# Kernel tuning notes

Measured on AMD Instinct MI355X. Metric: run time of the kernel, lower is better.

The kernel has to match this reference:

```python
import jax, jax.numpy as jnp
import numpy as np
import math

NUM_HEADS = 16
QK_NOPE = 128
QK_ROPE = 64
V_DIM = 128
Q_HEAD_DIM = QK_NOPE + QK_ROPE  # 192
KV_LORA = 512
ROPE_THETA = 10000.0
EPS = 1e-6


def setup_inputs() -> dict:
    key = jax.random.key(0)
    ks = jax.random.split(key, 8)
    B, S, H = 2, 2048, 2048
    hidden_states = jax.random.normal(ks[0], (B, S, H), dtype=jnp.float32)
    position_ids = jnp.broadcast_to(jnp.arange(S, dtype=jnp.int64), (B, S))
    attention_mask = jnp.broadcast_to(jnp.tril(jnp.ones((S, S), dtype=bool)), (B, 1, S, S))
    sc = 0.02
    w_q_down = jax.random.normal(ks[1], (1536, H), dtype=jnp.float32) * sc
    q_norm_w = jnp.ones((1536,), dtype=jnp.float32)
    w_q_up = jax.random.normal(ks[2], (NUM_HEADS * Q_HEAD_DIM, 1536), dtype=jnp.float32) * sc
    w_kv_down = jax.random.normal(ks[3], (KV_LORA + QK_ROPE, H), dtype=jnp.float32) * sc
    kv_norm_w = jnp.ones((KV_LORA,), dtype=jnp.float32)
    w_kv_up = jax.random.normal(ks[4], (NUM_HEADS * (QK_NOPE + V_DIM), KV_LORA), dtype=jnp.float32) * sc
    w_out = jax.random.normal(ks[5], (H, NUM_HEADS * V_DIM), dtype=jnp.float32) * sc
    return {"hidden_states": hidden_states, "position_ids": position_ids,
            "attention_mask": attention_mask, "w_q_down": w_q_down, "q_norm_w": q_norm_w,
            "w_q_up": w_q_up, "w_kv_down": w_kv_down, "kv_norm_w": kv_norm_w,
            "w_kv_up": w_kv_up, "w_out": w_out}


def rms_norm(x, w):
    xf = x.astype(jnp.float32)
    var = jnp.mean(xf * xf, axis=-1, keepdims=True)
    return w * (xf * jax.lax.rsqrt(var + EPS)).astype(x.dtype)


def rotate_half(x):
    d = x.shape[-1]
    return jnp.concatenate((-x[..., d // 2:], x[..., :d // 2]), axis=-1)


def _deinterleave(x):
    # torch: view(..., d//2, 2).transpose(-1,-2).reshape(..., d)
    d = x.shape[-1]
    return x.reshape(*x.shape[:-1], d // 2, 2).swapaxes(-1, -2).reshape(*x.shape[:-1], d)


def _rope_tables(seq_len, dtype):
    inv_freq = 1.0 / (ROPE_THETA ** (jnp.arange(0, QK_ROPE, 2, dtype=jnp.float32) / QK_ROPE))
    t = jnp.arange(seq_len, dtype=jnp.float32)
    freqs = jnp.outer(t, inv_freq)          # [S, QK_ROPE//2]
    emb = jnp.concatenate((freqs, freqs), axis=-1)  # [S, QK_ROPE]
    return jnp.cos(emb).astype(dtype), jnp.sin(emb).astype(dtype)


def mla_forward(hidden_states, position_ids, attention_mask,
                w_q_down, q_norm_w, w_q_up, w_kv_down, kv_norm_w, w_kv_up, w_out):
    B, S, H = hidden_states.shape
    # low-rank Q path
    q = hidden_states @ w_q_down.T                   # [B,S,1536]
    q = rms_norm(q, q_norm_w)
    q = q @ w_q_up.T                                 # [B,S,NH*192]
    q = q.reshape(B, S, NUM_HEADS, Q_HEAD_DIM).transpose(0, 2, 1, 3)  # [B,NH,S,192]
    q_nope, q_rope = q[..., :QK_NOPE], q[..., QK_NOPE:]
    # low-rank KV path
    c = hidden_states @ w_kv_down.T                  # [B,S,576]
    c_kv, k_rope = c[..., :KV_LORA], c[..., KV_LORA:]
    k_rope = k_rope.reshape(B, S, 1, QK_ROPE).transpose(0, 2, 1, 3)   # [B,1,S,64]
    kv = rms_norm(c_kv, kv_norm_w) @ w_kv_up.T       # [B,S,NH*(128+128)]
    kv = kv.reshape(B, S, NUM_HEADS, QK_NOPE + V_DIM).transpose(0, 2, 1, 3)
    k_nope, v = kv[..., :QK_NOPE], kv[..., QK_NOPE:]  # [B,NH,S,128] each
    # decoupled RoPE on the rope sub-dim
    cos, sin = _rope_tables(S, hidden_states.dtype)
    cos_p = cos[position_ids][:, None]               # [B,1,S,64]
    sin_p = sin[position_ids][:, None]
    qr = _deinterleave(q_rope)
    kr = _deinterleave(k_rope)
    q_rope = qr * cos_p + rotate_half(qr) * sin_p
    k_rope = kr * cos_p + rotate_half(kr) * sin_p
    query = jnp.concatenate([q_nope, q_rope], axis=-1)                      # [B,NH,S,192]
    key = jnp.concatenate([k_nope, jnp.broadcast_to(k_rope, (B, NUM_HEADS, S, QK_ROPE))], axis=-1)
    scores = jnp.einsum('bhqd,bhkd->bhqk', query, key) / math.sqrt(Q_HEAD_DIM)
    scores = jnp.where(attention_mask, scores, -jnp.inf)
    attn = jax.nn.softmax(scores, axis=-1).astype(query.dtype)              # [B,NH,S,S]
    out = jnp.einsum('bhqk,bhkd->bhqd', attn, v)                            # [B,NH,S,128]
    out = out.transpose(0, 2, 1, 3).reshape(B, S, NUM_HEADS * V_DIM)
    out = out @ w_out.T                                                     # [B,S,H]
    return out, attn


def reference(hidden_states, position_ids, attention_mask,
              w_q_down, q_norm_w, w_q_up, w_kv_down, kv_norm_w, w_kv_up, w_out):
    return mla_forward(hidden_states, position_ids, attention_mask,
                       w_q_down, q_norm_w, w_q_up, w_kv_down, kv_norm_w, w_kv_up, w_out)
```

## Files before the change

### kernel.cpp

```cpp
#include <hip/hip_runtime.h>
#include <hip/hip_bf16.h>
#include <math.h>

typedef unsigned short u16;
typedef unsigned int u32;
typedef __bf16 bf16x8 __attribute__((ext_vector_type(8)));
typedef float f32x4 __attribute__((ext_vector_type(4)));

__device__ __forceinline__ float bf2f(u16 h) {
    return __uint_as_float(((u32)h) << 16);
}
__device__ __forceinline__ u16 f2bf(float f) {
    u32 u = __float_as_uint(f);
    u32 r = (u + 0x7fffu + ((u >> 16) & 1u)) >> 16;
    return (u16)r;
}

__device__ __forceinline__ f32x4 mfma16(bf16x8 a, bf16x8 b, f32x4 c) {
    return __builtin_amdgcn_mfma_f32_16x16x32_bf16(a, b, c, 0, 0, 0);
}

__device__ __forceinline__ void g2l(const u16* g, u16* l) {
    __builtin_amdgcn_global_load_lds(
        (const __attribute__((address_space(1))) unsigned int*)g,
        (__attribute__((address_space(3))) unsigned int*)l,
        16, 0, 0);
}

struct DetectArgs {
    const void* p[8];
    int n[8];
};

__global__ __launch_bounds__(256) void detect_k(DetectArgs a, u32* flags) {
    int b = blockIdx.x;
    int t = threadIdx.x;
    const u16* p = (const u16*)a.p[b];
    u16 v = p[2 * t];
    int e = (v >> 7) & 0xff;
    bool insane = (e < 87) || (e > 167);
    unsigned long long m = __ballot(insane);
    __shared__ u32 s[4];
    int w = t >> 6;
    if ((t & 63) == 0) s[w] = (m != 0ull) ? 1u : 0u;
    __syncthreads();
    if (t == 0) flags[b] = s[0] | s[1] | s[2] | s[3];
}

__global__ __launch_bounds__(256) void convert_k(
    const void* src, u16* dst, int n, const u32* flags, int fi)
{
    u32 f = flags[fi];
    int j0 = blockIdx.x * 1024 + threadIdx.x * 4;
    if (f) {
        const float* s = (const float*)src;
        for (int k = 0; k < 4; k++) {
            int j = j0 + k;
            if (j < n) dst[j] = f2bf(s[j]);
        }
    } else {
        const u16* s = (const u16*)src;
        for (int k = 0; k < 4; k++) {
            int j = j0 + k;
            if (j < n) dst[j] = s[j];
        }
    }
}

__global__ __launch_bounds__(256) void gemm128(
    const u16* __restrict__ X, int xRow, long long xBat,
    const u16* __restrict__ W, int wRow, long long wBat,
    u16* __restrict__ Cb, float* __restrict__ Cf,
    int cRow, long long cBatB, long long cBatH,
    int N, int K)
{
    __shared__ __align__(16) u16 As[128 * 32];
    __shared__ __align__(16) u16 Bs[128 * 32];

    int z = blockIdx.z;
    const u16* Xz = X + (long long)z * xBat;
    const u16* Wz = W + (long long)z * wBat;
    long long cOff = (long long)(z >> 4) * cBatB + (long long)(z & 15) * cBatH;

    int t = threadIdx.x;
    int lane = t & 63, w = t >> 6;
    int sr = t >> 2;
    int sc = (t & 3) * 8;
    int m0 = blockIdx.y * 128, n0 = blockIdx.x * 128;
    int wr = (w >> 1) * 64, wc = (w & 1) * 64;
    int mrow = lane & 15, quad = lane >> 4;

    u16* As0 = &As[t * 8];
    u16* As1 = &As[2048 + t * 8];
    u16* Bs0 = &Bs[t * 8];
    u16* Bs1 = &Bs[2048 + t * 8];

    f32x4 zero = {0.f, 0.f, 0.f, 0.f};
    f32x4 acc[4][4];
    for (int i = 0; i < 4; i++)
        for (int j = 0; j < 4; j++) acc[i][j] = zero;

    for (int k0 = 0; k0 < K; k0 += 32) {
        const u16* ga0 = Xz + (long long)(m0 + sr) * xRow + k0 + sc;
        const u16* ga1 = ga0 + (long long)64 * xRow;
        int bn0 = n0 + sr;      if (bn0 >= N) bn0 = N - 1;
        int bn1 = n0 + sr + 64; if (bn1 >= N) bn1 = N - 1;
        const u16* gb0 = Wz + (long long)bn0 * wRow + k0 + sc;
        const u16* gb1 = Wz + (long long)bn1 * wRow + k0 + sc;
        __syncthreads();
        g2l(ga0, As0);
        g2l(ga1, As1);
        g2l(gb0, Bs0);
        g2l(gb1, Bs1);
        __syncthreads();

        bf16x8 af[4], bfr[4];
        for (int i = 0; i < 4; i++) {
            af[i]  = *(const bf16x8*)(&As[(wr + i * 16 + mrow) * 32 + quad * 8]);
            bfr[i] = *(const bf16x8*)(&Bs[(wc + i * 16 + mrow) * 32 + quad * 8]);
        }
        for (int mt = 0; mt < 4; mt++)
            for (int nt = 0; nt < 4; nt++)
                acc[mt][nt] = mfma16(af[mt], bfr[nt], acc[mt][nt]);
    }

    for (int mt = 0; mt < 4; mt++)
        for (int nt = 0; nt < 4; nt++)
            for (int r = 0; r < 4; r++) {
                int row = m0 + wr + mt * 16 + quad * 4 + r;
                int col = n0 + wc + nt * 16 + mrow;
                if (col < N) {
                    long long idx = cOff + (long long)row * cRow + col;
                    float v = acc[mt][nt][r];
                    if (Cb) Cb[idx] = f2bf(v); else Cf[idx] = v;
                }
            }
}

__global__ __launch_bounds__(256) void gemm128_xf32(
    const float* __restrict__ X, int xRow, long long xBat,
    const u16* __restrict__ W, int wRow, long long wBat,
    u16* __restrict__ Cb, int cRow, long long cBatB, long long cBatH,
    int N, int K)
{
    __shared__ __align__(16) u16 As[128 * 32];
    __shared__ __align__(16) u16 Bs[128 * 32];

    int z = blockIdx.z;
    const float* Xz = X + (long long)z * xBat;
    const u16* Wz = W + (long long)z * wBat;
    long long cOff = (long long)(z >> 4) * cBatB + (long long)(z & 15) * cBatH;

    int t = threadIdx.x;
    int lane = t & 63, w = t >> 6;
    int sr = t >> 2;
    int sc = (t & 3) * 8;
    int m0 = blockIdx.y * 128, n0 = blockIdx.x * 128;
    int wr = (w >> 1) * 64, wc = (w & 1) * 64;
    int mrow = lane & 15, quad = lane >> 4;

    u16* Bs0 = &Bs[t * 8];
    u16* Bs1 = &Bs[2048 + t * 8];

    f32x4 zero = {0.f, 0.f, 0.f, 0.f};
    f32x4 acc[4][4];
    for (int i = 0; i < 4; i++)
        for (int j = 0; j < 4; j++) acc[i][j] = zero;

    int kEnd = m0 + 128; if (kEnd > K) kEnd = K;

    for (int k0 = 0; k0 < kEnd; k0 += 32) {
        const float* ap0 = Xz + (long long)(m0 + sr) * xRow + k0 + sc;
        const float* ap1 = Xz + (long long)(m0 + sr + 64) * xRow + k0 + sc;
        float4 a0l = *(const float4*)(ap0), a0h = *(const float4*)(ap0 + 4);
        float4 a1l = *(const float4*)(ap1), a1h = *(const float4*)(ap1 + 4);
        int bn0 = n0 + sr;      if (bn0 >= N) bn0 = N - 1;
        int bn1 = n0 + sr + 64; if (bn1 >= N) bn1 = N - 1;
        const u16* gb0 = Wz + (long long)bn0 * wRow + k0 + sc;
        const u16* gb1 = Wz + (long long)bn1 * wRow + k0 + sc;
        u16 pa0[8] = {f2bf(a0l.x), f2bf(a0l.y), f2bf(a0l.z), f2bf(a0l.w),
                      f2bf(a0h.x), f2bf(a0h.y), f2bf(a0h.z), f2bf(a0h.w)};
        u16 pa1[8] = {f2bf(a1l.x), f2bf(a1l.y), f2bf(a1l.z), f2bf(a1l.w),
                      f2bf(a1h.x), f2bf(a1h.y), f2bf(a1h.z), f2bf(a1h.w)};
        __syncthreads();
        *(uint4*)(&As[sr * 32 + sc]) = *(const uint4*)pa0;
        *(uint4*)(&As[(sr + 64) * 32 + sc]) = *(const uint4*)pa1;
        g2l(gb0, Bs0);
        g2l(gb1, Bs1);
        __syncthreads();

        bf16x8 af[4], bfr[4];
        for (int i = 0; i < 4; i++) {
            af[i]  = *(const bf16x8*)(&As[(wr + i * 16 + mrow) * 32 + quad * 8]);
            bfr[i] = *(const bf16x8*)(&Bs[(wc + i * 16 + mrow) * 32 + quad * 8]);
        }
        for (int mt = 0; mt < 4; mt++)
            for (int nt = 0; nt < 4; nt++)
                acc[mt][nt] = mfma16(af[mt], bfr[nt], acc[mt][nt]);
    }

    for (int mt = 0; mt < 4; mt++)
        for (int nt = 0; nt < 4; nt++)
            for (int r = 0; r < 4; r++) {
                int row = m0 + wr + mt * 16 + quad * 4 + r;
                int col = n0 + wc + nt * 16 + mrow;
                if (col < N)
                    Cb[cOff + (long long)row * cRow + col] = f2bf(acc[mt][nt][r]);
            }
}

__global__ __launch_bounds__(256) void rmsnorm_k(
    const float* __restrict__ in, int inRow,
    const u16* __restrict__ wgt,
    u16* __restrict__ out, int outRow, int len)
{
    int row = blockIdx.x;
    const float* x = in + (long long)row * inRow;
    u16* o = out + (long long)row * outRow;
    int t = threadIdx.x;
    float ss = 0.f;
    for (int j = t; j < len; j += 256) { float v = x[j]; ss += v * v; }
    for (int s = 1; s < 64; s <<= 1) ss += __shfl_xor(ss, s);
    __shared__ float red[4];
    int w = t >> 6, lane = t & 63;
    if (lane == 0) red[w] = ss;
    __syncthreads();
    float tot = red[0] + red[1] + red[2] + red[3];
    float r = rsqrtf(tot / (float)len + 1e-6f);
    for (int j = t; j < len; j += 256)
        o[j] = f2bf(bf2f(wgt[j]) * (x[j] * r));
}

__device__ __forceinline__ void rope64(const float* xin, float* xo, int pos) {
    for (int i = 0; i < 32; i++) {
        float ex = (float)(2 * i) * (1.0f / 64.0f);
        float invf = expf(-ex * 9.210340371976184f);
        float ang = (float)pos * invf;
        float sn, cs;
        sincosf(ang, &sn, &cs);
        float a = xin[2 * i], b = xin[2 * i + 1];
        xo[i] = a * cs - b * sn;
        xo[32 + i] = b * cs + a * sn;
    }
}

__global__ __launch_bounds__(256) void rope_q_k(u16* __restrict__ qf) {
    int idx = blockIdx.x * 256 + threadIdx.x;
    int row = idx >> 4, h = idx & 15, pos = row & 2047;
    u16* p = qf + (long long)row * 3072 + h * 192 + 128;
    float xin[64], xo[64];
    for (int j = 0; j < 64; j++) xin[j] = bf2f(p[j]);
    rope64(xin, xo, pos);
    for (int j = 0; j < 64; j++) p[j] = f2bf(xo[j]);
}

__global__ __launch_bounds__(256) void rope_kk(
    const float* __restrict__ cpre, u16* __restrict__ kr) {
    int row = blockIdx.x * 256 + threadIdx.x;
    int pos = row & 2047;
    const float* src = cpre + (long long)row * 576 + 512;
    float xin[64], xo[64];
    for (int j = 0; j < 64; j++) xin[j] = src[j];
    rope64(xin, xo, pos);
    u16* dst = kr + (long long)row * 64;
    for (int j = 0; j < 64; j++) dst[j] = f2bf(xo[j]);
}

__global__ void transpose_v(const u16* __restrict__ kvup, u16* __restrict__ Vt) {
    __shared__ u16 tile[32][33];
    int bh = blockIdx.z, b = bh >> 4, h = bh & 15;
    int s0 = blockIdx.x * 32, d0 = blockIdx.y * 32;
    int tx = threadIdx.x, ty = threadIdx.y;
    for (int i = 0; i < 4; i++) {
        int s = s0 + ty + i * 8;
        tile[ty + i * 8][tx] = kvup[(long long)(b * 2048 + s) * 4096 + h * 256 + 128 + d0 + tx];
    }
    __syncthreads();
    for (int i = 0; i < 4; i++) {
        int d = d0 + ty + i * 8;
        Vt[((long long)bh * 128 + d) * 2048 + s0 + tx] = tile[tx][ty + i * 8];
    }
}

#define ATTN_SCALE 0.07216878364870323f

__global__ __launch_bounds__(256) void scores_gemm(
    const u16* __restrict__ qf, const u16* __restrict__ kvup,
    const u16* __restrict__ krope, float* __restrict__ attn)
{
    int n0 = blockIdx.x * 128, q0 = blockIdx.y * 128;
    if (n0 > q0) return;
    int bh = blockIdx.z, b = bh >> 4, h = bh & 15;
    const u16* qb = qf + (long long)b * 2048 * 3072 + h * 192;
    const u16* kn = kvup + (long long)b * 2048 * 4096 + h * 256;
    const u16* kr = krope + (long long)b * 2048 * 64;
    long long abase = (long long)bh * 4194304;

    __shared__ __align__(16) u16 As[128 * 32];
    __shared__ __align__(16) u16 Bs[128 * 32];
    int t = threadIdx.x, lane = t & 63, w = t >> 6;
    int sr = t >> 2, sc = (t & 3) * 8;
    int wr = (w >> 1) * 64, wc = (w & 1) * 64;
    int mrow = lane & 15, quad = lane >> 4;

    u16* As0 = &As[t * 8];
    u16* As1 = &As[2048 + t * 8];
    u16* Bs0 = &Bs[t * 8];
    u16* Bs1 = &Bs[2048 + t * 8];

    f32x4 zero = {0.f, 0.f, 0.f, 0.f};
    f32x4 acc[4][4];
    for (int i = 0; i < 4; i++)
        for (int j = 0; j < 4; j++) acc[i][j] = zero;

    for (int k0 = 0; k0 < 192; k0 += 32) {
        const u16* ga0 = qb + (long long)(q0 + sr) * 3072 + k0 + sc;
        const u16* ga1 = ga0 + (long long)64 * 3072;
        const u16 *gb0, *gb1;
        if (k0 < 128) {
            gb0 = kn + (long long)(n0 + sr) * 4096 + k0 + sc;
            gb1 = gb0 + (long long)64 * 4096;
        } else {
            gb0 = kr + (long long)(n0 + sr) * 64 + (k0 - 128) + sc;
            gb1 = gb0 + (long long)64 * 64;
        }
        __syncthreads();
        g2l(ga0, As0);
        g2l(ga1, As1);
        g2l(gb0, Bs0);
        g2l(gb1, Bs1);
        __syncthreads();

        bf16x8 af[4], bfr[4];
        for (int i = 0; i < 4; i++) {
            af[i]  = *(const bf16x8*)(&As[(wr + i * 16 + mrow) * 32 + quad * 8]);
            bfr[i] = *(const bf16x8*)(&Bs[(wc + i * 16 + mrow) * 32 + quad * 8]);
        }
        for (int mt = 0; mt < 4; mt++)
            for (int nt = 0; nt < 4; nt++)
                acc[mt][nt] = mfma16(af[mt], bfr[nt], acc[mt][nt]);
    }

    for (int mt = 0; mt < 4; mt++)
        for (int nt = 0; nt < 4; nt++)
            for (int r = 0; r < 4; r++) {
                int row = q0 + wr + mt * 16 + quad * 4 + r;
                int col = n0 + wc + nt * 16 + mrow;
                attn[abase + (long long)row * 2048 + col] = acc[mt][nt][r] * ATTN_SCALE;
            }
}

__global__ __launch_bounds__(256) void softmax_rows(float* __restrict__ attn) {
    int r = blockIdx.x;
    long long bh = blockIdx.y;
    float* p = attn + bh * 4194304LL + (long long)r * 2048;
    int t = threadIdx.x;
    int valid = r + 1;
    int j0 = t * 4;

    float v[8];
    float mx = -INFINITY;
#pragma unroll
    for (int h = 0; h < 2; h++) {
        int j = j0 + h * 1024;
        if (j + 4 <= valid) {
            float4 q = *(const float4*)(p + j);
            v[h * 4 + 0] = q.x; v[h * 4 + 1] = q.y;
            v[h * 4 + 2] = q.z; v[h * 4 + 3] = q.w;
        } else {
#pragma unroll
            for (int k = 0; k < 4; k++) {
                int jj = j + k;
                v[h * 4 + k] = (jj < valid) ? p[jj] : -INFINITY;
            }
        }
#pragma unroll
        for (int k = 0; k < 4; k++) mx = fmaxf(mx, v[h * 4 + k]);
    }
    for (int s = 1; s < 64; s <<= 1) mx = fmaxf(mx, __shfl_xor(mx, s));
    __shared__ float sm[4], s2[4];
    int w = t >> 6;
    if ((t & 63) == 0) sm[w] = mx;
    __syncthreads();
    mx = fmaxf(fmaxf(sm[0], sm[1]), fmaxf(sm[2], sm[3]));

    float ss = 0.f;
#pragma unroll
    for (int i = 0; i < 8; i++) {
        float e = (v[i] == -INFINITY) ? 0.f : expf(v[i] - mx);
        v[i] = e;
        ss += e;
    }
    for (int s = 1; s < 64; s <<= 1) ss += __shfl_xor(ss, s);
    if ((t & 63) == 0) s2[w] = ss;
    __syncthreads();
    ss = s2[0] + s2[1] + s2[2] + s2[3];
    float inv = 1.0f / ss;

#pragma unroll
    for (int h = 0; h < 2; h++) {
        float4 q;
        q.x = v[h * 4 + 0] * inv;
        q.y = v[h * 4 + 1] * inv;
        q.z = v[h * 4 + 2] * inv;
        q.w = v[h * 4 + 3] * inv;
        *(float4*)(p + j0 + h * 1024) = q;
    }
}

extern "C" void kernel_launch(void* const* d_in, const int* in_sizes, int n_in,
                              void* d_out, int out_size, void* d_ws, size_t ws_size,
                              hipStream_t stream) {
    (void)in_sizes; (void)n_in; (void)out_size; (void)ws_size;

    const void* r_hidden = d_in[0];
    const void* r_wqd    = d_in[3];
    const void* r_qnw    = d_in[4];
    const void* r_wqu    = d_in[5];
    const void* r_wkvd   = d_in[6];
    const void* r_kvnw   = d_in[7];
    const void* r_wkvu   = d_in[8];
    const void* r_wout   = d_in[9];

    float* out_p  = (float*)d_out;
    float* attn_p = (float*)d_out + 8388608LL;

    char* ws = (char*)d_ws;
    size_t off = 0;
    auto alloc = [&](size_t bytes) { void* p = ws + off; off = (off + bytes + 255) & ~(size_t)255; return p; };

    u32* flags = (u32*)alloc(256);
    char* regionA = (char*)alloc(25165824 + 9437184);
    float* q_pre = (float*)regionA;
    float* c_pre = (float*)(regionA + 25165824);
    u16* kv_up   = (u16*)regionA;
    char* regionB = (char*)alloc(16777216);
    u16* hidden_c = (u16*)regionB;
    u16* Vt       = (u16*)regionB;
    char* regionC = (char*)alloc(12582912);
    u16* q_c   = (u16*)regionC;
    u16* kv_c  = (u16*)regionC;
    u16* krope = (u16*)(regionC + 4194304);
    u16* wqd_c  = (u16*)alloc(1536LL * 2048 * 2);
    u16* qnw_c  = (u16*)alloc(1536LL * 2);
    u16* wqu_c  = (u16*)alloc(3072LL * 1536 * 2);
    u16* wkvd_c = (u16*)alloc(576LL * 2048 * 2);
    u16* kvnw_c = (u16*)alloc(512LL * 2);
    u16* wkvu_c = (u16*)alloc(4096LL * 512 * 2);
    u16* wout_c = (u16*)alloc(2048LL * 2048 * 2);
    u16* q_full = (u16*)alloc(4096LL * 3072 * 2);
    u16* Obuf   = q_full;

    DetectArgs da;
    da.p[0] = r_hidden; da.n[0] = 8388608;
    da.p[1] = r_wqd;    da.n[1] = 3145728;
    da.p[2] = r_qnw;    da.n[2] = 1536;
    da.p[3] = r_wqu;    da.n[3] = 4718592;
    da.p[4] = r_wkvd;   da.n[4] = 1179648;
    da.p[5] = r_kvnw;   da.n[5] = 512;
    da.p[6] = r_wkvu;   da.n[6] = 2097152;
    da.p[7] = r_wout;   da.n[7] = 4194304;
    hipLaunchKernelGGL(detect_k, dim3(8), dim3(256), 0, stream, da, flags);

    const void* srcs[8] = {r_hidden, r_wqd, r_qnw, r_wqu, r_wkvd, r_kvnw, r_wkvu, r_wout};
    u16* dsts[8] = {hidden_c, wqd_c, qnw_c, wqu_c, wkvd_c, kvnw_c, wkvu_c, wout_c};
    for (int i = 0; i < 8; i++) {
        int n = da.n[i];
        hipLaunchKernelGGL(convert_k, dim3((n + 1023) / 1024), dim3(256), 0, stream,
            srcs[i], dsts[i], n, flags, i);
    }

    hipLaunchKernelGGL(gemm128, dim3(12, 32, 1), dim3(256), 0, stream,
        hidden_c, 2048, 0LL, wqd_c, 2048, 0LL, (u16*)nullptr, q_pre, 1536, 0LL, 0LL, 1536, 2048);
    hipLaunchKernelGGL(rmsnorm_k, dim3(4096), dim3(256), 0, stream,
        q_pre, 1536, qnw_c, q_c, 1536, 1536);
    hipLaunchKernelGGL(gemm128, dim3(24, 32, 1), dim3(256), 0, stream,
        q_c, 1536, 0LL, wqu_c, 1536, 0LL, q_full, (float*)nullptr, 3072, 0LL, 0LL, 3072, 1536);
    hipLaunchKernelGGL(rope_q_k, dim3(256), dim3(256), 0, stream, q_full);
    hipLaunchKernelGGL(gemm128, dim3(5, 32, 1), dim3(256), 0, stream,
        hidden_c, 2048, 0LL, wkvd_c, 2048, 0LL, (u16*)nullptr, c_pre, 576, 0LL, 0LL, 576, 2048);
    hipLaunchKernelGGL(rmsnorm_k, dim3(4096), dim3(256), 0, stream,
        c_pre, 576, kvnw_c, kv_c, 512, 512);
    hipLaunchKernelGGL(rope_kk, dim3(16), dim3(256), 0, stream, c_pre, krope);
    hipLaunchKernelGGL(gemm128, dim3(32, 32, 1), dim3(256), 0, stream,
        kv_c, 512, 0LL, wkvu_c, 512, 0LL, kv_up, (float*)nullptr, 4096, 0LL, 0LL, 4096, 512);
    hipLaunchKernelGGL(transpose_v, dim3(64, 4, 32), dim3(32, 8), 0, stream, kv_up, Vt);
    hipLaunchKernelGGL(scores_gemm, dim3(16, 16, 32), dim3(256), 0, stream,
        q_full, kv_up, krope, attn_p);
    hipLaunchKernelGGL(softmax_rows, dim3(2048, 32), dim3(256), 0, stream, attn_p);
    hipLaunchKernelGGL(gemm128_xf32, dim3(1, 16, 32), dim3(256), 0, stream,
        attn_p, 2048, 4194304LL, Vt, 2048, 262144LL, Obuf,
        2048, 4194304LL, 128LL, 128, 2048);
    hipLaunchKernelGGL(gemm128, dim3(16, 32, 1), dim3(256), 0, stream,
        Obuf, 2048, 0LL, wout_c, 2048, 0LL, (u16*)nullptr, out_p, 2048, 0LL, 0LL, 2048, 2048);
}
```

Baseline: 1.317 ms.

## Batch converts, merge down-projections and up-projections, zero masked tiles in scores kernel

Replaces the eight conversion launches with one kernel that looks up its segment by block index. Concatenates the q and kv down-projection weights into one GEMM, fuses both RMSNorms into one launch, and runs both up-projection GEMMs in a single dual launch. The scores kernel now writes zeros for fully masked tiles, and softmax stores only the columns up to the causal tile boundary, so the attention matrix is written once instead of twice. Also reverses row order in the attn@V GEMM so the long causal rows are scheduled first, and vectorises the rope loads and stores. The cost is extra workspace aliasing and more branching inside the combined kernels.

```diff
diff --git a/kernel.cpp b/kernel.cpp
--- a/kernel.cpp
+++ b/kernel.cpp
@@ -47,11 +47,23 @@
     if (t == 0) flags[b] = s[0] | s[1] | s[2] | s[3];
 }
 
-__global__ __launch_bounds__(256) void convert_k(
-    const void* src, u16* dst, int n, const u32* flags, int fi)
-{
-    u32 f = flags[fi];
-    int j0 = blockIdx.x * 1024 + threadIdx.x * 4;
+struct ConvArgs {
+    const void* src[8];
+    u16* dst[8];
+    int n[8];
+    int pre[9];
+};
+
+__global__ __launch_bounds__(256) void convert_all(ConvArgs a, const u32* flags) {
+    int bx = blockIdx.x;
+    int i = 0;
+    while (i < 7 && bx >= a.pre[i + 1]) i++;
+    int lb = bx - a.pre[i];
+    int n = a.n[i];
+    u32 f = flags[i];
+    const void* src = a.src[i];
+    u16* dst = a.dst[i];
+    int j0 = lb * 1024 + threadIdx.x * 4;
     if (f) {
         const float* s = (const float*)src;
         for (int k = 0; k < 4; k++) {
@@ -137,6 +149,73 @@
             }
 }
 
+struct DualGemm {
+    const u16* X[2]; int xRow[2];
+    const u16* W[2]; int wRow[2];
+    u16* C[2];       int cRow[2];
+    int N[2]; int K[2]; int xmax[2];
+};
+
+__global__ __launch_bounds__(256) void gemm128_dual(DualGemm d) {
+    int s = blockIdx.z;
+    if ((int)blockIdx.x >= d.xmax[s]) return;
+    const u16* __restrict__ X = d.X[s]; int xRow = d.xRow[s];
+    const u16* __restrict__ W = d.W[s]; int wRow = d.wRow[s];
+    u16* __restrict__ Cb = d.C[s];      int cRow = d.cRow[s];
+    int N = d.N[s], K = d.K[s];
+
+    __shared__ __align__(16) u16 As[128 * 32];
+    __shared__ __align__(16) u16 Bs[128 * 32];
+
+    int t = threadIdx.x;
+    int lane = t & 63, w = t >> 6;
+    int sr = t >> 2;
+    int sc = (t & 3) * 8;
+    int m0 = blockIdx.y * 128, n0 = blockIdx.x * 128;
+    int wr = (w >> 1) * 64, wc = (w & 1) * 64;
+    int mrow = lane & 15, quad = lane >> 4;
+
+    u16* As0 = &As[t * 8];
+    u16* As1 = &As[2048 + t * 8];
+    u16* Bs0 = &Bs[t * 8];
+    u16* Bs1 = &Bs[2048 + t * 8];
+
+    f32x4 zero = {0.f, 0.f, 0.f, 0.f};
+    f32x4 acc[4][4];
+    for (int i = 0; i < 4; i++)
+        for (int j = 0; j < 4; j++) acc[i][j] = zero;
+
+    for (int k0 = 0; k0 < K; k0 += 32) {
+        const u16* ga0 = X + (long long)(m0 + sr) * xRow + k0 + sc;
+        const u16* ga1 = ga0 + (long long)64 * xRow;
+        const u16* gb0 = W + (long long)(n0 + sr) * wRow + k0 + sc;
+        const u16* gb1 = gb0 + (long long)64 * wRow;
+        __syncthreads();
+        g2l(ga0, As0);
+        g2l(ga1, As1);
+        g2l(gb0, Bs0);
+        g2l(gb1, Bs1);
+        __syncthreads();
+
+        bf16x8 af[4], bfr[4];
+        for (int i = 0; i < 4; i++) {
+            af[i]  = *(const bf16x8*)(&As[(wr + i * 16 + mrow) * 32 + quad * 8]);
+            bfr[i] = *(const bf16x8*)(&Bs[(wc + i * 16 + mrow) * 32 + quad * 8]);
+        }
+        for (int mt = 0; mt < 4; mt++)
+            for (int nt = 0; nt < 4; nt++)
+                acc[mt][nt] = mfma16(af[mt], bfr[nt], acc[mt][nt]);
+    }
+
+    for (int mt = 0; mt < 4; mt++)
+        for (int nt = 0; nt < 4; nt++)
+            for (int r = 0; r < 4; r++) {
+                int row = m0 + wr + mt * 16 + quad * 4 + r;
+                int col = n0 + wc + nt * 16 + mrow;
+                Cb[(long long)row * cRow + col] = f2bf(acc[mt][nt][r]);
+            }
+}
+
 __global__ __launch_bounds__(256) void gemm128_xf32(
     const float* __restrict__ X, int xRow, long long xBat,
     const u16* __restrict__ W, int wRow, long long wBat,
@@ -155,7 +234,8 @@
     int lane = t & 63, w = t >> 6;
     int sr = t >> 2;
     int sc = (t & 3) * 8;
-    int m0 = blockIdx.y * 128, n0 = blockIdx.x * 128;
+    int m0 = ((int)gridDim.y - 1 - (int)blockIdx.y) * 128;
+    int n0 = blockIdx.x * 128;
     int wr = (w >> 1) * 64, wc = (w & 1) * 64;
     int mrow = lane & 15, quad = lane >> 4;
 
@@ -209,14 +289,23 @@
             }
 }
 
-__global__ __launch_bounds__(256) void rmsnorm_k(
-    const float* __restrict__ in, int inRow,
-    const u16* __restrict__ wgt,
-    u16* __restrict__ out, int outRow, int len)
+__global__ __launch_bounds__(256) void rmsnorm2_k(
+    const float* __restrict__ base,
+    const u16* __restrict__ qw, const u16* __restrict__ kw,
+    u16* __restrict__ qo, u16* __restrict__ ko)
 {
     int row = blockIdx.x;
-    const float* x = in + (long long)row * inRow;
-    u16* o = out + (long long)row * outRow;
+    const float* x;
+    const u16* wgt;
+    u16* o;
+    int len;
+    if (blockIdx.y == 0) {
+        x = base + (long long)row * 2112;       wgt = qw;
+        o = qo + (long long)row * 1536;         len = 1536;
+    } else {
+        x = base + (long long)row * 2112 + 1536; wgt = kw;
+        o = ko + (long long)row * 512;          len = 512;
+    }
     int t = threadIdx.x;
     float ss = 0.f;
     for (int j = t; j < len; j += 256) { float v = x[j]; ss += v * v; }
@@ -248,22 +337,33 @@
     int idx = blockIdx.x * 256 + threadIdx.x;
     int row = idx >> 4, h = idx & 15, pos = row & 2047;
     u16* p = qf + (long long)row * 3072 + h * 192 + 128;
+    uint4 vv[8];
+    for (int j = 0; j < 8; j++) vv[j] = ((const uint4*)p)[j];
+    const u16* xb = (const u16*)vv;
     float xin[64], xo[64];
-    for (int j = 0; j < 64; j++) xin[j] = bf2f(p[j]);
+    for (int j = 0; j < 64; j++) xin[j] = bf2f(xb[j]);
     rope64(xin, xo, pos);
-    for (int j = 0; j < 64; j++) p[j] = f2bf(xo[j]);
+    uint4 ov[8];
+    u16* ob = (u16*)ov;
+    for (int j = 0; j < 64; j++) ob[j] = f2bf(xo[j]);
+    for (int j = 0; j < 8; j++) ((uint4*)p)[j] = ov[j];
 }
 
 __global__ __launch_bounds__(256) void rope_kk(
-    const float* __restrict__ cpre, u16* __restrict__ kr) {
+    const float* __restrict__ base, u16* __restrict__ kr) {
     int row = blockIdx.x * 256 + threadIdx.x;
     int pos = row & 2047;
-    const float* src = cpre + (long long)row * 576 + 512;
-    float xin[64], xo[64];
-    for (int j = 0; j < 64; j++) xin[j] = src[j];
+    const float* src = base + (long long)row * 2112 + 2048;
+    float4 fv[16];
+    for (int j = 0; j < 16; j++) fv[j] = ((const float4*)src)[j];
+    const float* xin = (const float*)fv;
+    float xo[64];
     rope64(xin, xo, pos);
-    u16* dst = kr + (long long)row * 64;
-    for (int j = 0; j < 64; j++) dst[j] = f2bf(xo[j]);
+    uint4 ov[8];
+    u16* ob = (u16*)ov;
+    for (int j = 0; j < 64; j++) ob[j] = f2bf(xo[j]);
+    uint4* dst = (uint4*)(kr + (long long)row * 64);
+    for (int j = 0; j < 8; j++) dst[j] = ov[j];
 }
 
 __global__ void transpose_v(const u16* __restrict__ kvup, u16* __restrict__ Vt) {
@@ -289,16 +389,29 @@
     const u16* __restrict__ krope, float* __restrict__ attn)
 {
     int n0 = blockIdx.x * 128, q0 = blockIdx.y * 128;
-    if (n0 > q0) return;
-    int bh = blockIdx.z, b = bh >> 4, h = bh & 15;
+    int bh = blockIdx.z;
+    long long abase = (long long)bh * 4194304;
+    int t = threadIdx.x;
+
+    if (n0 > q0) {
+        float4 z4 = {0.f, 0.f, 0.f, 0.f};
+        for (int k = 0; k < 16; k++) {
+            int fo = t + k * 256;
+            int tr = fo >> 5;
+            int tc = (fo & 31) * 4;
+            *(float4*)(attn + abase + (long long)(q0 + tr) * 2048 + n0 + tc) = z4;
+        }
+        return;
+    }
+
+    int b = bh >> 4, h = bh & 15;
     const u16* qb = qf + (long long)b * 2048 * 3072 + h * 192;
     const u16* kn = kvup + (long long)b * 2048 * 4096 + h * 256;
     const u16* kr = krope + (long long)b * 2048 * 64;
-    long long abase = (long long)bh * 4194304;
 
     __shared__ __align__(16) u16 As[128 * 32];
     __shared__ __align__(16) u16 Bs[128 * 32];
-    int t = threadIdx.x, lane = t & 63, w = t >> 6;
+    int lane = t & 63, w = t >> 6;
     int sr = t >> 2, sc = (t & 3) * 8;
     int wr = (w >> 1) * 64, wc = (w & 1) * 64;
     int mrow = lane & 15, quad = lane >> 4;
@@ -356,6 +469,7 @@
     float* p = attn + bh * 4194304LL + (long long)r * 2048;
     int t = threadIdx.x;
     int valid = r + 1;
+    int B = ((r >> 7) + 1) << 7;
     int j0 = t * 4;
 
     float v[8];
@@ -399,12 +513,15 @@
 
 #pragma unroll
     for (int h = 0; h < 2; h++) {
-        float4 q;
-        q.x = v[h * 4 + 0] * inv;
-        q.y = v[h * 4 + 1] * inv;
-        q.z = v[h * 4 + 2] * inv;
-        q.w = v[h * 4 + 3] * inv;
-        *(float4*)(p + j0 + h * 1024) = q;
+        int j = j0 + h * 1024;
+        if (j < B) {
+            float4 q;
+            q.x = v[h * 4 + 0] * inv;
+            q.y = v[h * 4 + 1] * inv;
+            q.z = v[h * 4 + 2] * inv;
+            q.w = v[h * 4 + 3] * inv;
+            *(float4*)(p + j) = q;
+        }
     }
 }
 
@@ -430,21 +547,19 @@
     auto alloc = [&](size_t bytes) { void* p = ws + off; off = (off + bytes + 255) & ~(size_t)255; return p; };
 
     u32* flags = (u32*)alloc(256);
-    char* regionA = (char*)alloc(25165824 + 9437184);
-    float* q_pre = (float*)regionA;
-    float* c_pre = (float*)(regionA + 25165824);
-    u16* kv_up   = (u16*)regionA;
+    char* regionA = (char*)alloc(34603008);
+    float* qc_pre = (float*)regionA;
+    u16* kv_up    = (u16*)regionA;
     char* regionB = (char*)alloc(16777216);
     u16* hidden_c = (u16*)regionB;
+    u16* kv_c     = (u16*)regionB;
     u16* Vt       = (u16*)regionB;
     char* regionC = (char*)alloc(12582912);
     u16* q_c   = (u16*)regionC;
-    u16* kv_c  = (u16*)regionC;
-    u16* krope = (u16*)(regionC + 4194304);
-    u16* wqd_c  = (u16*)alloc(1536LL * 2048 * 2);
+    u16* wdown_c = (u16*)alloc(2112LL * 2048 * 2);
+    u16* krope = wdown_c;
     u16* qnw_c  = (u16*)alloc(1536LL * 2);
     u16* wqu_c  = (u16*)alloc(3072LL * 1536 * 2);
-    u16* wkvd_c = (u16*)alloc(576LL * 2048 * 2);
     u16* kvnw_c = (u16*)alloc(512LL * 2);
     u16* wkvu_c = (u16*)alloc(4096LL * 512 * 2);
     u16* wout_c = (u16*)alloc(2048LL * 2048 * 2);
@@ -462,28 +577,31 @@
     da.p[7] = r_wout;   da.n[7] = 4194304;
     hipLaunchKernelGGL(detect_k, dim3(8), dim3(256), 0, stream, da, flags);
 
-    const void* srcs[8] = {r_hidden, r_wqd, r_qnw, r_wqu, r_wkvd, r_kvnw, r_wkvu, r_wout};
-    u16* dsts[8] = {hidden_c, wqd_c, qnw_c, wqu_c, wkvd_c, kvnw_c, wkvu_c, wout_c};
-    for (int i = 0; i < 8; i++) {
-        int n = da.n[i];
-        hipLaunchKernelGGL(convert_k, dim3((n + 1023) / 1024), dim3(256), 0, stream,
-            srcs[i], dsts[i], n, flags, i);
-    }
-
-    hipLaunchKernelGGL(gemm128, dim3(12, 32, 1), dim3(256), 0, stream,
-        hidden_c, 2048, 0LL, wqd_c, 2048, 0LL, (u16*)nullptr, q_pre, 1536, 0LL, 0LL, 1536, 2048);
-    hipLaunchKernelGGL(rmsnorm_k, dim3(4096), dim3(256), 0, stream,
-        q_pre, 1536, qnw_c, q_c, 1536, 1536);
-    hipLaunchKernelGGL(gemm128, dim3(24, 32, 1), dim3(256), 0, stream,
-        q_c, 1536, 0LL, wqu_c, 1536, 0LL, q_full, (float*)nullptr, 3072, 0LL, 0LL, 3072, 1536);
+    ConvArgs ca;
+    ca.src[0] = r_hidden; ca.dst[0] = hidden_c;            ca.n[0] = 8388608;
+    ca.src[1] = r_wqd;    ca.dst[1] = wdown_c;             ca.n[1] = 3145728;
+    ca.src[2] = r_qnw;    ca.dst[2] = qnw_c;               ca.n[2] = 1536;
+    ca.src[3] = r_wqu;    ca.dst[3] = wqu_c;               ca.n[3] = 4718592;
+    ca.src[4] = r_wkvd;   ca.dst[4] = wdown_c + 3145728;   ca.n[4] = 1179648;
+    ca.src[5] = r_kvnw;   ca.dst[5] = kvnw_c;              ca.n[5] = 512;
+    ca.src[6] = r_wkvu;   ca.dst[6] = wkvu_c;              ca.n[6] = 2097152;
+    ca.src[7] = r_wout;   ca.dst[7] = wout_c;              ca.n[7] = 4194304;
+    ca.pre[0] = 0;
+    for (int i = 0; i < 8; i++) ca.pre[i + 1] = ca.pre[i] + (ca.n[i] + 1023) / 1024;
+    hipLaunchKernelGGL(convert_all, dim3(ca.pre[8]), dim3(256), 0, stream, ca, flags);
+
+    hipLaunchKernelGGL(gemm128, dim3(17, 32, 1), dim3(256), 0, stream,
+        hidden_c, 2048, 0LL, wdown_c, 2048, 0LL, (u16*)nullptr, qc_pre, 2112, 0LL, 0LL, 2112, 2048);
+    hipLaunchKernelGGL(rmsnorm2_k, dim3(4096, 2), dim3(256), 0, stream,
+        qc_pre, qnw_c, kvnw_c, q_c, kv_c);
+    hipLaunchKernelGGL(rope_kk, dim3(16), dim3(256), 0, stream, qc_pre, krope);
+    DualGemm dg;
+    dg.X[0] = q_c;   dg.xRow[0] = 1536; dg.W[0] = wqu_c;  dg.wRow[0] = 1536;
+    dg.C[0] = q_full; dg.cRow[0] = 3072; dg.N[0] = 3072;  dg.K[0] = 1536; dg.xmax[0] = 24;
+    dg.X[1] = kv_c;  dg.xRow[1] = 512;  dg.W[1] = wkvu_c; dg.wRow[1] = 512;
+    dg.C[1] = kv_up; dg.cRow[1] = 4096; dg.N[1] = 4096;   dg.K[1] = 512;  dg.xmax[1] = 32;
+    hipLaunchKernelGGL(gemm128_dual, dim3(32, 32, 2), dim3(256), 0, stream, dg);
     hipLaunchKernelGGL(rope_q_k, dim3(256), dim3(256), 0, stream, q_full);
-    hipLaunchKernelGGL(gemm128, dim3(5, 32, 1), dim3(256), 0, stream,
-        hidden_c, 2048, 0LL, wkvd_c, 2048, 0LL, (u16*)nullptr, c_pre, 576, 0LL, 0LL, 576, 2048);
-    hipLaunchKernelGGL(rmsnorm_k, dim3(4096), dim3(256), 0, stream,
-        c_pre, 576, kvnw_c, kv_c, 512, 512);
-    hipLaunchKernelGGL(rope_kk, dim3(16), dim3(256), 0, stream, c_pre, krope);
-    hipLaunchKernelGGL(gemm128, dim3(32, 32, 1), dim3(256), 0, stream,
-        kv_c, 512, 0LL, wkvu_c, 512, 0LL, kv_up, (float*)nullptr, 4096, 0LL, 0LL, 4096, 512);
     hipLaunchKernelGGL(transpose_v, dim3(64, 4, 32), dim3(32, 8), 0, stream, kv_up, Vt);
     hipLaunchKernelGGL(scores_gemm, dim3(16, 16, 32), dim3(256), 0, stream,
         q_full, kv_up, krope, attn_p);
```

Result: faster. 1.261 ms (-4.3%).
